# Optimization experiments

Hardware: AMD Instinct MI355X
Metric: run time of the kernel (lower is better)

Reference implementation:

```python
import jax, jax.numpy as jnp
import numpy as np

B, S, HID = 2, 2048, 2048
H, D_NOPE, D_ROPE, D_V, R = 16, 128, 64, 128, 512
D_Q = D_NOPE + D_ROPE  # 192
MAX_POS = 4096
EPS = 1e-6


def setup_inputs() -> dict:
    key = jax.random.key(0)
    ks = jax.random.split(key, 10)
    hidden_states = jax.random.normal(ks[0], (B, S, HID), dtype=jnp.float32)
    cos = jax.random.uniform(ks[1], (MAX_POS, D_ROPE // 2), dtype=jnp.float32)
    sin = jax.random.uniform(ks[2], (MAX_POS, D_ROPE // 2), dtype=jnp.float32)
    position_ids = jnp.arange(B * S, dtype=jnp.int64).reshape(B, S)
    sc = lambda d: 1.0 / np.sqrt(d)
    Wq = jax.random.normal(ks[3], (HID, H * D_Q), dtype=jnp.float32) * sc(HID)
    Wkv_a = jax.random.normal(ks[4], (HID, R + D_ROPE), dtype=jnp.float32) * sc(HID)
    ln_g = jnp.ones((R,), dtype=jnp.float32)
    ln_b = jnp.zeros((R,), dtype=jnp.float32)
    Wkv_b = jax.random.normal(ks[5], (R, H * (D_NOPE + D_V)), dtype=jnp.float32) * sc(R)
    Wo = jax.random.normal(ks[6], (H * D_V, HID), dtype=jnp.float32) * sc(H * D_V)
    return {"hidden_states": hidden_states, "cos": cos, "sin": sin,
            "position_ids": position_ids, "Wq": Wq, "Wkv_a": Wkv_a,
            "ln_g": ln_g, "ln_b": ln_b, "Wkv_b": Wkv_b, "Wo": Wo}


def _rope(t, cos, sin, position_ids):
    # t: [B,S,Hh,D_ROPE]; cos/sin: [MAX_POS, D_ROPE//2]
    c = cos[position_ids]  # [B,S,D_ROPE//2]
    s = sin[position_ids]
    c2 = jnp.concatenate([c, c], axis=-1)[:, :, None, :]  # [B,S,1,D_ROPE]
    s2 = jnp.concatenate([s, s], axis=-1)[:, :, None, :]
    half = t.shape[-1] // 2
    x1, x2 = t[..., :half], t[..., half:]
    rot = jnp.concatenate([-x2, x1], axis=-1)
    return t * c2 + rot * s2


def reference(hidden_states, cos, sin, position_ids, Wq, Wkv_a, ln_g, ln_b, Wkv_b, Wo):
    b, s, _ = hidden_states.shape
    # Q projection -> split nope/rope parts
    q = (hidden_states @ Wq).reshape(b, s, H, D_Q)
    q_nope, q_pe = q[..., :D_NOPE], q[..., D_NOPE:]
    q_pe = _rope(q_pe, cos, sin, position_ids)
    query = jnp.concatenate([q_nope, q_pe], axis=-1)  # [B,S,H,192]

    # KV latent projection
    ckv = hidden_states @ Wkv_a  # [B,S,R+D_ROPE]
    kv_c, k_pe = ckv[..., :R], ckv[..., R:]
    mu = jnp.mean(kv_c, axis=-1, keepdims=True)
    var = jnp.mean(jnp.square(kv_c - mu), axis=-1, keepdims=True)
    kv_c_n = (kv_c - mu) * jax.lax.rsqrt(var + EPS) * ln_g + ln_b
    k_pe = _rope(k_pe[:, :, None, :], cos, sin, position_ids)[:, :, 0, :]  # [B,S,64]

    # Expand latent -> per-head k_nope / v
    kv = (kv_c_n @ Wkv_b).reshape(b, s, H, D_NOPE + D_V)
    k_nope, v = kv[..., :D_NOPE], kv[..., D_NOPE:]
    key = jnp.concatenate(
        [k_nope, jnp.broadcast_to(k_pe[:, :, None, :], (b, s, H, D_ROPE))], axis=-1)

    scale = D_Q ** -0.5
    scores = jnp.einsum('bqhd,bkhd->bhqk', query, key) * scale
    causal = jnp.tril(jnp.ones((s, s), dtype=bool))
    scores = jnp.where(causal[None, None], scores, jnp.finfo(scores.dtype).min)
    attn = jax.nn.softmax(scores, axis=-1)
    out = jnp.einsum('bhqk,bkhd->bqhd', attn, v).reshape(b, s, H * D_V)
    return out @ Wo
```

## Files before the change

kernel.cpp:

```cpp
#include <hip/hip_runtime.h>
#include <math.h>
#include <stdint.h>

#define B_      2
#define S_      2048
#define HID_    2048
#define H_      16
#define D_NOPE_ 128
#define D_ROPE_ 64
#define D_V_    128
#define R_      512
#define D_Q_    192
#define NTOK    (B_ * S_)
#define EPS_    1e-6f

typedef __attribute__((ext_vector_type(8))) short bf16x8;
typedef __attribute__((ext_vector_type(4))) float f32x4;

__device__ __forceinline__ short f2bf(float x) {
    union { float f; unsigned u; } un; un.f = x;
    unsigned r = (un.u + 0x7fffu + ((un.u >> 16) & 1u)) >> 16;
    return (short)r;
}
__device__ __forceinline__ float bf2f(short s) {
    union { unsigned u; float f; } un;
    un.u = ((unsigned)(unsigned short)s) << 16;
    return un.f;
}

__device__ __forceinline__ void async_ld16(const short* gsrc, short* ldst) {
    __builtin_amdgcn_global_load_lds(
        (const __attribute__((address_space(1))) void*)gsrc,
        (__attribute__((address_space(3))) void*)ldst, 16, 0, 0);
}

#define BARX() { __builtin_amdgcn_sched_barrier(0); __builtin_amdgcn_s_barrier(); __builtin_amdgcn_sched_barrier(0); }

__global__ __launch_bounds__(256) void castk(const float* __restrict__ in, short* __restrict__ out) {
    int i = blockIdx.x * 256 + threadIdx.x;
    float4 v = ((const float4*)in)[i];
    ushort4 o;
    o.x = (unsigned short)f2bf(v.x); o.y = (unsigned short)f2bf(v.y);
    o.z = (unsigned short)f2bf(v.z); o.w = (unsigned short)f2bf(v.w);
    ((ushort4*)out)[i] = o;
}

__global__ __launch_bounds__(256) void transpose_cast(const float* __restrict__ W,
                                                      short* __restrict__ WT,
                                                      int K, int Nreal) {
    __shared__ float T[32][33];
    const int n0 = blockIdx.x * 32, k0 = blockIdx.y * 32;
    const int t = threadIdx.x;
    const int r = t >> 3, c4 = (t & 7) * 4;
    float4 v = make_float4(0.f, 0.f, 0.f, 0.f);
    if (n0 < Nreal) v = *(const float4*)&W[(size_t)(k0 + r) * Nreal + n0 + c4];
    T[r][c4 + 0] = v.x; T[r][c4 + 1] = v.y; T[r][c4 + 2] = v.z; T[r][c4 + 3] = v.w;
    __syncthreads();
    const int n = t >> 3, k4 = (t & 7) * 4;
    ushort4 o;
    o.x = (unsigned short)f2bf(T[k4 + 0][n]);
    o.y = (unsigned short)f2bf(T[k4 + 1][n]);
    o.z = (unsigned short)f2bf(T[k4 + 2][n]);
    o.w = (unsigned short)f2bf(T[k4 + 3][n]);
    *(ushort4*)&WT[(size_t)(n0 + n) * K + k0 + k4] = o;
}

template <int OUTBF>
__global__ __launch_bounds__(256) void gemm_mfma(const short* __restrict__ A,
                                                 const short* __restrict__ BT,
                                                 void* __restrict__ C,
                                                 int M, int N, int K) {
    __shared__ short As[128 * 32];
    __shared__ short Bs[128 * 32];
    const int tid = threadIdx.x;
    const int lane = tid & 63, w = tid >> 6;
    const int brow = blockIdx.y * 128, bcol = blockIdx.x * 128;

    const int o0 = w * 1024 + lane * 16;
    const int r0 = o0 >> 6, q0p = (o0 >> 4) & 3;
    const int o1 = o0 + 4096;
    const int r1 = o1 >> 6, q1p = (o1 >> 4) & 3;
    const int s0 = r0 * K + 8 * (q0p ^ ((r0 >> 1) & 3));
    const int s1 = r1 * K + 8 * (q1p ^ ((r1 >> 1) & 3));
    const short* Ab = A + (size_t)brow * K;
    const short* Bb = BT + (size_t)bcol * K;
    short* AsU0 = &As[w * 512]; short* AsU1 = &As[w * 512 + 2048];
    short* BsU0 = &Bs[w * 512]; short* BsU1 = &Bs[w * 512 + 2048];

    const int wr = w >> 1, wc = w & 1;
    const int c16 = lane & 15, g = lane >> 4;
    const int qph = (g ^ ((c16 >> 1) & 3)) * 8;

    f32x4 zero = {0.f, 0.f, 0.f, 0.f};
    f32x4 acc[4][4];
#pragma unroll
    for (int i = 0; i < 4; ++i)
#pragma unroll
        for (int j = 0; j < 4; ++j) acc[i][j] = zero;

    for (int k0 = 0; k0 < K; k0 += 32) {
        async_ld16(Ab + s0 + k0, AsU0);
        async_ld16(Ab + s1 + k0, AsU1);
        async_ld16(Bb + s0 + k0, BsU0);
        async_ld16(Bb + s1 + k0, BsU1);
        __syncthreads();
        bf16x8 af[4], bf[4];
#pragma unroll
        for (int i = 0; i < 4; ++i) {
            af[i] = *(const bf16x8*)&As[(wr * 64 + i * 16 + c16) * 32 + qph];
            bf[i] = *(const bf16x8*)&Bs[(wc * 64 + i * 16 + c16) * 32 + qph];
        }
#pragma unroll
        for (int mi = 0; mi < 4; ++mi)
#pragma unroll
            for (int ni = 0; ni < 4; ++ni)
                acc[mi][ni] = __builtin_amdgcn_mfma_f32_16x16x32_bf16(af[mi], bf[ni], acc[mi][ni], 0, 0, 0);
        __syncthreads();
    }

#pragma unroll
    for (int mi = 0; mi < 4; ++mi)
#pragma unroll
        for (int ni = 0; ni < 4; ++ni)
#pragma unroll
            for (int reg = 0; reg < 4; ++reg) {
                int row = brow + wr * 64 + mi * 16 + 4 * g + reg;
                int col = bcol + wc * 64 + ni * 16 + c16;
                if (OUTBF) ((short*)C)[(size_t)row * N + col] = f2bf(acc[mi][ni][reg]);
                else       ((float*)C)[(size_t)row * N + col] = acc[mi][ni][reg];
            }
}

template <int QA>
__global__ __launch_bounds__(512) void gemm8(const short* __restrict__ A,
                                             const short* __restrict__ BT,
                                             void* __restrict__ C0,
                                             float* __restrict__ C1,
                                             int N, int K, int nbx) {
    __shared__ short LB[2][4][8192];

    const int tid = threadIdx.x, lane = tid & 63, w = tid >> 6;
    const int c16 = lane & 15, g = lane >> 4;
    const int wr = w >> 2, wc = w & 3;
    const int qph = (g ^ ((c16 >> 1) & 3)) * 8;

    const int nwg = gridDim.x;
    const int swz = (blockIdx.x & 7) * (nwg >> 3) + (blockIdx.x >> 3);
    const int brow = (swz / nbx) * 256, bcol = (swz % nbx) * 256;

    const int o0 = w * 1024 + lane * 16;
    const int o1 = o0 + 8192;
    const int r0 = o0 >> 6, lc0 = ((o0 >> 4) & 3) ^ ((r0 >> 1) & 3);
    const int r1 = o1 >> 6, lc1 = ((o1 >> 4) & 3) ^ ((r1 >> 1) & 3);
    const short* aS0 = A + (size_t)(brow + r0) * K + lc0 * 8;
    const short* aS1 = A + (size_t)(brow + r1) * K + lc1 * 8;
    const short* bS0 = BT + (size_t)(bcol + r0) * K + lc0 * 8;
    const short* bS1 = BT + (size_t)(bcol + r1) * K + lc1 * 8;
    const int d0 = w * 512, d1 = 4096 + w * 512;

    f32x4 zero = {0.f, 0.f, 0.f, 0.f};
    f32x4 acc[8][4];
#pragma unroll
    for (int i = 0; i < 8; ++i)
#pragma unroll
        for (int j = 0; j < 4; ++j) acc[i][j] = zero;

    const int NT = K >> 6;
    async_ld16(aS0,      &LB[0][0][d0]);  async_ld16(aS1,      &LB[0][0][d1]);
    async_ld16(aS0 + 32, &LB[0][1][d0]);  async_ld16(aS1 + 32, &LB[0][1][d1]);
    async_ld16(bS0,      &LB[0][2][d0]);  async_ld16(bS1,      &LB[0][2][d1]);
    async_ld16(bS0 + 32, &LB[0][3][d0]);  async_ld16(bS1 + 32, &LB[0][3][d1]);
    asm volatile("s_waitcnt vmcnt(0)" ::: "memory");
    BARX();

    int cur = 0;
    const int arb = wr * 128, brb = wc * 64;
    for (int kt = 0; kt < NT; ++kt) {
        const bool stg = (kt + 1 < NT);
        const int ko = (kt + 1) * 64;
        short (*CB)[8192] = LB[cur];
        short (*NB)[8192] = LB[cur ^ 1];
        bf16x8 af[4], bf[4];

#pragma unroll
        for (int ni = 0; ni < 4; ++ni)
            bf[ni] = *(const bf16x8*)&CB[2][(brb + ni * 16 + c16) * 32 + qph];
#pragma unroll
        for (int mi = 0; mi < 4; ++mi)
            af[mi] = *(const bf16x8*)&CB[0][(arb + mi * 16 + c16) * 32 + qph];
        if (stg) { async_ld16(aS0 + ko, &NB[0][d0]); async_ld16(aS1 + ko, &NB[0][d1]); }
        BARX();
        __builtin_amdgcn_s_setprio(1);
#pragma unroll
        for (int mi = 0; mi < 4; ++mi)
#pragma unroll
            for (int ni = 0; ni < 4; ++ni)
                acc[mi][ni] = __builtin_amdgcn_mfma_f32_16x16x32_bf16(af[mi], bf[ni], acc[mi][ni], 0, 0, 0);
        __builtin_amdgcn_s_setprio(0);
        BARX();

#pragma unroll
        for (int mi = 0; mi < 4; ++mi)
            af[mi] = *(const bf16x8*)&CB[0][(arb + 64 + mi * 16 + c16) * 32 + qph];
        if (stg) {
            async_ld16(bS0 + ko, &NB[2][d0]); async_ld16(bS1 + ko, &NB[2][d1]);
            asm volatile("s_waitcnt vmcnt(4)" ::: "memory");
        } else {
            asm volatile("s_waitcnt vmcnt(0)" ::: "memory");
        }
        BARX();
        __builtin_amdgcn_s_setprio(1);
#pragma unroll
        for (int mi = 0; mi < 4; ++mi)
#pragma unroll
            for (int ni = 0; ni < 4; ++ni)
                acc[4 + mi][ni] = __builtin_amdgcn_mfma_f32_16x16x32_bf16(af[mi], bf[ni], acc[4 + mi][ni], 0, 0, 0);
        __builtin_amdgcn_s_setprio(0);
        BARX();

#pragma unroll
        for (int ni = 0; ni < 4; ++ni)
            bf[ni] = *(const bf16x8*)&CB[3][(brb + ni * 16 + c16) * 32 + qph];
#pragma unroll
        for (int mi = 0; mi < 4; ++mi)
            af[mi] = *(const bf16x8*)&CB[1][(arb + mi * 16 + c16) * 32 + qph];
        if (stg) { async_ld16(aS0 + ko + 32, &NB[1][d0]); async_ld16(aS1 + ko + 32, &NB[1][d1]); }
        BARX();
        __builtin_amdgcn_s_setprio(1);
#pragma unroll
        for (int mi = 0; mi < 4; ++mi)
#pragma unroll
            for (int ni = 0; ni < 4; ++ni)
                acc[mi][ni] = __builtin_amdgcn_mfma_f32_16x16x32_bf16(af[mi], bf[ni], acc[mi][ni], 0, 0, 0);
        __builtin_amdgcn_s_setprio(0);
        BARX();

#pragma unroll
        for (int mi = 0; mi < 4; ++mi)
            af[mi] = *(const bf16x8*)&CB[1][(arb + 64 + mi * 16 + c16) * 32 + qph];
        if (stg) {
            async_ld16(bS0 + ko + 32, &NB[3][d0]); async_ld16(bS1 + ko + 32, &NB[3][d1]);
            asm volatile("s_waitcnt vmcnt(4)" ::: "memory");
        }
        BARX();
        __builtin_amdgcn_s_setprio(1);
#pragma unroll
        for (int mi = 0; mi < 4; ++mi)
#pragma unroll
            for (int ni = 0; ni < 4; ++ni)
                acc[4 + mi][ni] = __builtin_amdgcn_mfma_f32_16x16x32_bf16(af[mi], bf[ni], acc[4 + mi][ni], 0, 0, 0);
        __builtin_amdgcn_s_setprio(0);
        BARX();

        cur ^= 1;
    }

    if (QA) {
        const int wcol = bcol + wc * 64;
        if (wcol < 3072) {
            short* qb = (short*)C0;
#pragma unroll
            for (int mi = 0; mi < 8; ++mi)
#pragma unroll
                for (int ni = 0; ni < 4; ++ni)
#pragma unroll
                    for (int reg = 0; reg < 4; ++reg) {
                        int row = brow + wr * 128 + mi * 16 + 4 * g + reg;
                        int col = wcol + ni * 16 + c16;
                        qb[(size_t)row * 3072 + col] = f2bf(acc[mi][ni][reg]);
                    }
        } else if (wcol < 3712) {
#pragma unroll
            for (int mi = 0; mi < 8; ++mi)
#pragma unroll
                for (int ni = 0; ni < 4; ++ni)
#pragma unroll
                    for (int reg = 0; reg < 4; ++reg) {
                        int row = brow + wr * 128 + mi * 16 + 4 * g + reg;
                        int col = wcol - 3072 + ni * 16 + c16;
                        C1[(size_t)row * 640 + col] = acc[mi][ni][reg];
                    }
        }
    } else {
        short* cc = (short*)C0;
#pragma unroll
        for (int mi = 0; mi < 8; ++mi)
#pragma unroll
            for (int ni = 0; ni < 4; ++ni)
#pragma unroll
                for (int reg = 0; reg < 4; ++reg) {
                    int row = brow + wr * 128 + mi * 16 + 4 * g + reg;
                    int col = bcol + wc * 64 + ni * 16 + c16;
                    cc[(size_t)row * N + col] = f2bf(acc[mi][ni][reg]);
                }
    }
}

__global__ __launch_bounds__(256) void rope_q_ip(short* __restrict__ qb,
                                                 const float* __restrict__ cosT,
                                                 const float* __restrict__ sinT,
                                                 const int* __restrict__ pid) {
    int gidx = blockIdx.x * 256 + threadIdx.x;
    int i = gidx & 31;
    int h = (gidx >> 5) & (H_ - 1);
    int tok = gidx >> 9;
    int pos = pid[tok];
    float c = cosT[pos * 32 + i];
    float s = sinT[pos * 32 + i];
    short* base = qb + (size_t)tok * (H_ * D_Q_) + h * D_Q_ + D_NOPE_;
    float x1 = bf2f(base[i]);
    float x2 = bf2f(base[i + 32]);
    base[i]      = f2bf(x1 * c - x2 * s);
    base[i + 32] = f2bf(x2 * c + x1 * s);
}

__global__ __launch_bounds__(256) void ln_rope(const float* __restrict__ ckv,
                                               const float* __restrict__ gam,
                                               const float* __restrict__ bet,
                                               const float* __restrict__ cosT,
                                               const float* __restrict__ sinT,
                                               const int* __restrict__ pid,
                                               short* __restrict__ kvcn,
                                               short* __restrict__ kpe) {
    const int tok = blockIdx.x, tid = threadIdx.x;
    const float* x = ckv + (size_t)tok * 640;
    float v0 = x[tid], v1 = x[tid + 256];
    float s = v0 + v1, sq = v0 * v0 + v1 * v1;
#pragma unroll
    for (int m = 1; m < 64; m <<= 1) { s += __shfl_xor(s, m); sq += __shfl_xor(sq, m); }
    __shared__ float ws[8];
    int wid = tid >> 6, lane = tid & 63;
    if (lane == 0) { ws[wid] = s; ws[4 + wid] = sq; }
    __syncthreads();
    s = ws[0] + ws[1] + ws[2] + ws[3];
    sq = ws[4] + ws[5] + ws[6] + ws[7];
    float mean = s * (1.f / 512.f);
    float var = sq * (1.f / 512.f) - mean * mean;
    float rstd = rsqrtf(var + EPS_);
    kvcn[(size_t)tok * 512 + tid]       = f2bf((v0 - mean) * rstd * gam[tid] + bet[tid]);
    kvcn[(size_t)tok * 512 + tid + 256] = f2bf((v1 - mean) * rstd * gam[tid + 256] + bet[tid + 256]);
    if (tid < 32) {
        int pos = pid[tok];
        float c = cosT[pos * 32 + tid], sn = sinT[pos * 32 + tid];
        float x1 = x[512 + tid], x2 = x[512 + 32 + tid];
        kpe[(size_t)tok * 64 + tid]      = f2bf(x1 * c - x2 * sn);
        kpe[(size_t)tok * 64 + 32 + tid] = f2bf(x2 * c + x1 * sn);
    }
}

__global__ __launch_bounds__(256) void transpose_v(const short* __restrict__ kvb,
                                                   short* __restrict__ Vt) {
    __shared__ short T[64][72];
    const int s0 = blockIdx.x * 64, d0 = blockIdx.y * 64, bh = blockIdx.z;
    const int b = bh >> 4, h = bh & 15;
    const int t = threadIdx.x;
    const int r = t >> 3, c8 = (t & 7) * 8;
#pragma unroll
    for (int i = 0; i < 2; ++i) {
        int rr = r + 32 * i;
        bf16x8 v = *(const bf16x8*)&kvb[((size_t)(b * 2048 + s0 + rr) * 16 + h) * 256 + 128 + d0 + c8];
        *(bf16x8*)&T[rr][c8] = v;
    }
    __syncthreads();
#pragma unroll
    for (int i = 0; i < 2; ++i) {
        int d = r + 32 * i;
        bf16x8 o;
#pragma unroll
        for (int j = 0; j < 8; ++j) o[j] = T[c8 + j][d];
        *(bf16x8*)&Vt[((size_t)(b * 16 + h) * 128 + d0 + d) * 2048 + s0 + c8] = o;
    }
}

__global__ __launch_bounds__(256) void flash_mfma(const short* __restrict__ qb,
                                                  const short* __restrict__ kvb,
                                                  const short* __restrict__ kpe,
                                                  const short* __restrict__ Vt,
                                                  short* __restrict__ attno) {
    __shared__ short Ks[2][64 * 128];
    __shared__ short Vs[2][128 * 64];
    __shared__ short P[4][16][72];

    const int flat = blockIdx.x;
    const int xcd = flat & 7, idx = flat >> 3;
    const int bh = xcd + 8 * (idx >> 4);
    const int pair = idx & 15;
    const int b = bh >> 4, h = bh & 15;

    const int tid = threadIdx.x, lane = tid & 63, w = tid >> 6;
    const int c16 = lane & 15, g = lane >> 4, g8 = g * 8;
    const float SC2 = 0.10412063f;

    const int o = w * 1024 + lane * 16;
    const int rK = o >> 8, ccK = ((o >> 4) & 15) ^ (rK & 7);
    const int rV = o >> 7, ccV = ((o >> 4) & 7) ^ (rV & 7);
    const short* kB0  = kvb + ((size_t)((b * 2048 + rK) * 16 + h)) * 256 + ccK * 8;
    const short* vB0  = Vt + ((size_t)((b * 16 + h) * 128 + rV)) * 2048 + ccV * 8;
    const short* peB0 = kpe + (size_t)(b * 2048 + c16) * 64 + g8;

    f32x4 zero = {0.f, 0.f, 0.f, 0.f};

#define STAGE(BUF)                                                                  \
    {                                                                               \
        _Pragma("unroll")                                                           \
        for (int rnd = 0; rnd < 4; ++rnd)                                           \
            async_ld16(kRun + (size_t)rnd * 65536,                                  \
                       &Ks[BUF][(rnd * 4096 + w * 1024) >> 1]);                     \
        _Pragma("unroll")                                                           \
        for (int rnd = 0; rnd < 4; ++rnd)                                           \
            async_ld16(vRun + (size_t)rnd * 65536,                                  \
                       &Vs[BUF][(rnd * 4096 + w * 1024) >> 1]);                     \
        kRun += 64 * 4096;                                                          \
        vRun += 64;                                                                 \
    }

    for (int half = 0; half < 2; ++half) {
        const int qt = half ? (31 - pair) : pair;
        const int q0 = qt * 64;
        const int qrow = q0 + w * 16;

        const size_t qbase = ((size_t)(b * 2048 + qrow + c16) * 16 + h) * 192 + g8;
        bf16x8 qf[6];
#pragma unroll
        for (int ks = 0; ks < 6; ++ks) qf[ks] = *(const bf16x8*)(qb + qbase + 32 * ks);

        f32x4 acc[8];
#pragma unroll
        for (int i = 0; i < 8; ++i) acc[i] = zero;
        float mreg[4] = {-INFINITY, -INFINITY, -INFINITY, -INFINITY};
        float lreg[4] = {0.f, 0.f, 0.f, 0.f};

        const short* kRun = kB0;
        const short* vRun = vB0;
        const short* peRun = peB0;

        const int nt = qt + 1;
        STAGE(0);
        __syncthreads();
        int cur = 0;

        for (int kt = 0; kt < nt; ++kt) {
            if (kt + 1 < nt) STAGE(cur ^ 1);

            f32x4 sc[4];
#pragma unroll
            for (int i = 0; i < 4; ++i) sc[i] = zero;

            __builtin_amdgcn_s_setprio(1);
#pragma unroll
            for (int ks = 0; ks < 4; ++ks)
#pragma unroll
                for (int nb = 0; nb < 4; ++nb) {
                    int row = nb * 16 + c16;
                    bf16x8 kf = *(const bf16x8*)&Ks[cur][row * 128 + (((g + 4 * ks) ^ (row & 7)) << 3)];
                    sc[nb] = __builtin_amdgcn_mfma_f32_16x16x32_bf16(qf[ks], kf, sc[nb], 0, 0, 0);
                }
#pragma unroll
            for (int ks = 0; ks < 2; ++ks)
#pragma unroll
                for (int nb = 0; nb < 4; ++nb) {
                    bf16x8 kf = *(const bf16x8*)(peRun + (size_t)nb * 16 * 64 + ks * 32);
                    sc[nb] = __builtin_amdgcn_mfma_f32_16x16x32_bf16(qf[4 + ks], kf, sc[nb], 0, 0, 0);
                }
            __builtin_amdgcn_s_setprio(0);
            peRun += 64 * 64;

            if (kt == nt - 1) {
#pragma unroll
                for (int nb = 0; nb < 4; ++nb)
#pragma unroll
                    for (int reg = 0; reg < 4; ++reg) {
                        int col = (nt - 1) * 64 + nb * 16 + c16;
                        int row = qrow + 4 * g + reg;
                        if (col > row) sc[nb][reg] = -INFINITY;
                    }
            }

            float rmax[4];
#pragma unroll
            for (int reg = 0; reg < 4; ++reg)
                rmax[reg] = fmaxf(fmaxf(sc[0][reg], sc[1][reg]), fmaxf(sc[2][reg], sc[3][reg]));
#pragma unroll
            for (int m = 1; m < 16; m <<= 1)
#pragma unroll
                for (int reg = 0; reg < 4; ++reg)
                    rmax[reg] = fmaxf(rmax[reg], __shfl_xor(rmax[reg], m));

            float grow = rmax[0] * SC2 - mreg[0];
#pragma unroll
            for (int reg = 1; reg < 4; ++reg) grow = fmaxf(grow, rmax[reg] * SC2 - mreg[reg]);
            if (__any(grow > 8.f)) {
#pragma unroll
                for (int reg = 0; reg < 4; ++reg) {
                    float mnew = fmaxf(mreg[reg], rmax[reg] * SC2);
                    float alpha = exp2f(mreg[reg] - mnew);
                    mreg[reg] = mnew;
                    lreg[reg] *= alpha;
#pragma unroll
                    for (int nb = 0; nb < 8; ++nb) acc[nb][reg] *= alpha;
                }
            }

#pragma unroll
            for (int reg = 0; reg < 4; ++reg) {
                float p0 = exp2f(fmaf(sc[0][reg], SC2, -mreg[reg]));
                float p1 = exp2f(fmaf(sc[1][reg], SC2, -mreg[reg]));
                float p2 = exp2f(fmaf(sc[2][reg], SC2, -mreg[reg]));
                float p3 = exp2f(fmaf(sc[3][reg], SC2, -mreg[reg]));
                sc[0][reg] = p0; sc[1][reg] = p1; sc[2][reg] = p2; sc[3][reg] = p3;
                lreg[reg] += (p0 + p1) + (p2 + p3);
            }

#pragma unroll
            for (int nb = 0; nb < 4; ++nb)
#pragma unroll
                for (int reg = 0; reg < 4; ++reg)
                    P[w][4 * g + reg][nb * 16 + c16] = f2bf(sc[nb][reg]);

            __builtin_amdgcn_s_setprio(1);
#pragma unroll
            for (int ks = 0; ks < 2; ++ks) {
                bf16x8 pf = *(const bf16x8*)&P[w][c16][ks * 32 + g8];
#pragma unroll
                for (int nb = 0; nb < 8; ++nb) {
                    int row = nb * 16 + c16;
                    bf16x8 vf = *(const bf16x8*)&Vs[cur][row * 64 + (((g + 4 * ks) ^ (row & 7)) << 3)];
                    acc[nb] = __builtin_amdgcn_mfma_f32_16x16x32_bf16(pf, vf, acc[nb], 0, 0, 0);
                }
            }
            __builtin_amdgcn_s_setprio(0);

            __syncthreads();
            cur ^= 1;
        }

#pragma unroll
        for (int m = 1; m < 16; m <<= 1)
#pragma unroll
            for (int reg = 0; reg < 4; ++reg)
                lreg[reg] += __shfl_xor(lreg[reg], m);
        float inv[4];
#pragma unroll
        for (int reg = 0; reg < 4; ++reg) inv[reg] = 1.f / lreg[reg];
#pragma unroll
        for (int nb = 0; nb < 8; ++nb)
#pragma unroll
            for (int reg = 0; reg < 4; ++reg)
                attno[((size_t)(b * 2048 + qrow + 4 * g + reg) * 16 + h) * 128 + nb * 16 + c16] =
                    f2bf(acc[nb][reg] * inv[reg]);
    }
#undef STAGE
}

extern "C" void kernel_launch(void* const* d_in, const int* in_sizes, int n_in,
                              void* d_out, int out_size, void* d_ws, size_t ws_size,
                              hipStream_t stream) {
    const float* hidden = (const float*)d_in[0];
    const float* cosT   = (const float*)d_in[1];
    const float* sinT   = (const float*)d_in[2];
    const int*   pid    = (const int*)d_in[3];
    const float* Wq     = (const float*)d_in[4];
    const float* Wkv_a  = (const float*)d_in[5];
    const float* ln_g   = (const float*)d_in[6];
    const float* ln_b   = (const float*)d_in[7];
    const float* Wkv_b  = (const float*)d_in[8];
    const float* Wo     = (const float*)d_in[9];
    float* out = (float*)d_out;

    char* p = (char*)d_ws;
    short* hid_bf = (short*)p;               p += (size_t)NTOK * 2048 * 2;
    short* WqkaT  = (short*)p;               p += (size_t)3840 * 2048 * 2;
    short* WkbT   = (short*)p;               p += (size_t)4096 * 512 * 2;
    short* WoT    = (short*)p;               p += (size_t)2048 * 2048 * 2;
    char*  big    = p;                       p += (size_t)NTOK * 3072 * 4;
    short* qbuf   = (short*)p;               p += (size_t)NTOK * 3072 * 2;
    short* kvcn   = (short*)p;               p += (size_t)NTOK * 512 * 2;
    short* kpe    = (short*)p;               p += (size_t)NTOK * 64 * 2;
    short* kvb    = (short*)p;               p += (size_t)NTOK * 4096 * 2;

    float* ckv   = (float*)big;
    short* Vt    = (short*)(big + (size_t)NTOK * 640 * 4);
    short* attno = (short*)(big + (size_t)NTOK * 640 * 4 + (size_t)2 * 16 * 128 * 2048 * 2);

    castk<<<8192, 256, 0, stream>>>(hidden, hid_bf);
    transpose_cast<<<dim3(96, 64), 256, 0, stream>>>(Wq, WqkaT, 2048, 3072);
    transpose_cast<<<dim3(24, 64), 256, 0, stream>>>(Wkv_a, WqkaT + (size_t)3072 * 2048, 2048, 576);
    transpose_cast<<<dim3(128, 16), 256, 0, stream>>>(Wkv_b, WkbT, 512, 4096);
    transpose_cast<<<dim3(64, 64), 256, 0, stream>>>(Wo, WoT, 2048, 2048);

    gemm8<1><<<240, 512, 0, stream>>>(hid_bf, WqkaT, qbuf, ckv, 3840, 2048, 15);
    rope_q_ip<<<(NTOK * H_ * 32) / 256, 256, 0, stream>>>(qbuf, cosT, sinT, pid);
    ln_rope<<<NTOK, 256, 0, stream>>>(ckv, ln_g, ln_b, cosT, sinT, pid, kvcn, kpe);
    gemm8<0><<<256, 512, 0, stream>>>(kvcn, WkbT, kvb, nullptr, 4096, 512, 16);
    transpose_v<<<dim3(32, 2, 32), 256, 0, stream>>>(kvb, Vt);
    flash_mfma<<<512, 256, 0, stream>>>(qbuf, kvb, kpe, Vt, attno);
    gemm_mfma<0><<<dim3(16, 32), 256, 0, stream>>>(attno, WoT, out, 4096, 2048, 2048);
}
```

Before: 308.2 us.

## Replace output-projection GEMM with double-buffered 512-thread pipelined kernel

Swaps the simple 128x128-tile, single-buffered output-projection GEMM for a new 128x256-tile kernel with 8 waves. It double-buffers LDS, prefetches the next K tile with async loads while MFMAs run, and raises wave priority around the MFMA blocks. Block indices are swizzled across the grid of 256 workgroups. The goal is to hide global-load latency and cut barrier stalls in the final GEMM, at the cost of more LDS use and a fixed layout that assumes M divisible by 128 and N by 256.

```diff
diff --git a/kernel.cpp b/kernel.cpp
--- a/kernel.cpp
+++ b/kernel.cpp
@@ -65,72 +65,6 @@
     *(ushort4*)&WT[(size_t)(n0 + n) * K + k0 + k4] = o;
 }
 
-template <int OUTBF>
-__global__ __launch_bounds__(256) void gemm_mfma(const short* __restrict__ A,
-                                                 const short* __restrict__ BT,
-                                                 void* __restrict__ C,
-                                                 int M, int N, int K) {
-    __shared__ short As[128 * 32];
-    __shared__ short Bs[128 * 32];
-    const int tid = threadIdx.x;
-    const int lane = tid & 63, w = tid >> 6;
-    const int brow = blockIdx.y * 128, bcol = blockIdx.x * 128;
-
-    const int o0 = w * 1024 + lane * 16;
-    const int r0 = o0 >> 6, q0p = (o0 >> 4) & 3;
-    const int o1 = o0 + 4096;
-    const int r1 = o1 >> 6, q1p = (o1 >> 4) & 3;
-    const int s0 = r0 * K + 8 * (q0p ^ ((r0 >> 1) & 3));
-    const int s1 = r1 * K + 8 * (q1p ^ ((r1 >> 1) & 3));
-    const short* Ab = A + (size_t)brow * K;
-    const short* Bb = BT + (size_t)bcol * K;
-    short* AsU0 = &As[w * 512]; short* AsU1 = &As[w * 512 + 2048];
-    short* BsU0 = &Bs[w * 512]; short* BsU1 = &Bs[w * 512 + 2048];
-
-    const int wr = w >> 1, wc = w & 1;
-    const int c16 = lane & 15, g = lane >> 4;
-    const int qph = (g ^ ((c16 >> 1) & 3)) * 8;
-
-    f32x4 zero = {0.f, 0.f, 0.f, 0.f};
-    f32x4 acc[4][4];
-#pragma unroll
-    for (int i = 0; i < 4; ++i)
-#pragma unroll
-        for (int j = 0; j < 4; ++j) acc[i][j] = zero;
-
-    for (int k0 = 0; k0 < K; k0 += 32) {
-        async_ld16(Ab + s0 + k0, AsU0);
-        async_ld16(Ab + s1 + k0, AsU1);
-        async_ld16(Bb + s0 + k0, BsU0);
-        async_ld16(Bb + s1 + k0, BsU1);
-        __syncthreads();
-        bf16x8 af[4], bf[4];
-#pragma unroll
-        for (int i = 0; i < 4; ++i) {
-            af[i] = *(const bf16x8*)&As[(wr * 64 + i * 16 + c16) * 32 + qph];
-            bf[i] = *(const bf16x8*)&Bs[(wc * 64 + i * 16 + c16) * 32 + qph];
-        }
-#pragma unroll
-        for (int mi = 0; mi < 4; ++mi)
-#pragma unroll
-            for (int ni = 0; ni < 4; ++ni)
-                acc[mi][ni] = __builtin_amdgcn_mfma_f32_16x16x32_bf16(af[mi], bf[ni], acc[mi][ni], 0, 0, 0);
-        __syncthreads();
-    }
-
-#pragma unroll
-    for (int mi = 0; mi < 4; ++mi)
-#pragma unroll
-        for (int ni = 0; ni < 4; ++ni)
-#pragma unroll
-            for (int reg = 0; reg < 4; ++reg) {
-                int row = brow + wr * 64 + mi * 16 + 4 * g + reg;
-                int col = bcol + wc * 64 + ni * 16 + c16;
-                if (OUTBF) ((short*)C)[(size_t)row * N + col] = f2bf(acc[mi][ni][reg]);
-                else       ((float*)C)[(size_t)row * N + col] = acc[mi][ni][reg];
-            }
-}
-
 template <int QA>
 __global__ __launch_bounds__(512) void gemm8(const short* __restrict__ A,
                                              const short* __restrict__ BT,
@@ -294,6 +228,117 @@
                     cc[(size_t)row * N + col] = f2bf(acc[mi][ni][reg]);
                 }
     }
+}
+
+__global__ __launch_bounds__(512) void gemm8n(const short* __restrict__ A,
+                                              const short* __restrict__ BT,
+                                              float* __restrict__ C,
+                                              int N, int K, int nbx) {
+    __shared__ short LA[2][2][4096];
+    __shared__ short LBt[2][2][8192];
+
+    const int tid = threadIdx.x, lane = tid & 63, w = tid >> 6;
+    const int c16 = lane & 15, g = lane >> 4;
+    const int wr = w >> 2, wc = w & 3;
+    const int qph = (g ^ ((c16 >> 1) & 3)) * 8;
+
+    const int nwg = gridDim.x;
+    const int swz = (blockIdx.x & 7) * (nwg >> 3) + (blockIdx.x >> 3);
+    const int brow = (swz / nbx) * 128, bcol = (swz % nbx) * 256;
+
+    const int oA = tid * 16;
+    const int rA = oA >> 6, lcA = ((oA >> 4) & 3) ^ ((rA >> 1) & 3);
+    const short* aS = A + (size_t)(brow + rA) * K + lcA * 8;
+    const int dA = oA >> 1;
+
+    const int o0 = w * 1024 + lane * 16, o1 = o0 + 8192;
+    const int r0 = o0 >> 6, lc0 = ((o0 >> 4) & 3) ^ ((r0 >> 1) & 3);
+    const int r1 = o1 >> 6, lc1 = ((o1 >> 4) & 3) ^ ((r1 >> 1) & 3);
+    const short* bS0 = BT + (size_t)(bcol + r0) * K + lc0 * 8;
+    const short* bS1 = BT + (size_t)(bcol + r1) * K + lc1 * 8;
+    const int d0 = o0 >> 1, d1 = o1 >> 1;
+
+    f32x4 zero = {0.f, 0.f, 0.f, 0.f};
+    f32x4 acc[4][4];
+#pragma unroll
+    for (int i = 0; i < 4; ++i)
+#pragma unroll
+        for (int j = 0; j < 4; ++j) acc[i][j] = zero;
+
+    const int NT = K >> 6;
+    async_ld16(aS,      &LA[0][0][dA]);
+    async_ld16(aS + 32, &LA[0][1][dA]);
+    async_ld16(bS0,      &LBt[0][0][d0]); async_ld16(bS1,      &LBt[0][0][d1]);
+    async_ld16(bS0 + 32, &LBt[0][1][d0]); async_ld16(bS1 + 32, &LBt[0][1][d1]);
+    asm volatile("s_waitcnt vmcnt(0)" ::: "memory");
+    BARX();
+
+    int cur = 0;
+    const int arb = wr * 64, brb = wc * 64;
+    for (int kt = 0; kt < NT; ++kt) {
+        const bool stg = (kt + 1 < NT);
+        const int ko = (kt + 1) * 64;
+        bf16x8 af[4], bf[4];
+
+#pragma unroll
+        for (int mi = 0; mi < 4; ++mi)
+            af[mi] = *(const bf16x8*)&LA[cur][0][(arb + mi * 16 + c16) * 32 + qph];
+#pragma unroll
+        for (int ni = 0; ni < 4; ++ni)
+            bf[ni] = *(const bf16x8*)&LBt[cur][0][(brb + ni * 16 + c16) * 32 + qph];
+        if (stg) {
+            async_ld16(aS + ko, &LA[cur ^ 1][0][dA]);
+            async_ld16(bS0 + ko, &LBt[cur ^ 1][0][d0]);
+            async_ld16(bS1 + ko, &LBt[cur ^ 1][0][d1]);
+            asm volatile("s_waitcnt vmcnt(3)" ::: "memory");
+        } else {
+            asm volatile("s_waitcnt vmcnt(0)" ::: "memory");
+        }
+        BARX();
+        __builtin_amdgcn_s_setprio(1);
+#pragma unroll
+        for (int mi = 0; mi < 4; ++mi)
+#pragma unroll
+            for (int ni = 0; ni < 4; ++ni)
+                acc[mi][ni] = __builtin_amdgcn_mfma_f32_16x16x32_bf16(af[mi], bf[ni], acc[mi][ni], 0, 0, 0);
+        __builtin_amdgcn_s_setprio(0);
+        BARX();
+
+#pragma unroll
+        for (int mi = 0; mi < 4; ++mi)
+            af[mi] = *(const bf16x8*)&LA[cur][1][(arb + mi * 16 + c16) * 32 + qph];
+#pragma unroll
+        for (int ni = 0; ni < 4; ++ni)
+            bf[ni] = *(const bf16x8*)&LBt[cur][1][(brb + ni * 16 + c16) * 32 + qph];
+        if (stg) {
+            async_ld16(aS + ko + 32, &LA[cur ^ 1][1][dA]);
+            async_ld16(bS0 + ko + 32, &LBt[cur ^ 1][1][d0]);
+            async_ld16(bS1 + ko + 32, &LBt[cur ^ 1][1][d1]);
+            asm volatile("s_waitcnt vmcnt(3)" ::: "memory");
+        }
+        BARX();
+        __builtin_amdgcn_s_setprio(1);
+#pragma unroll
+        for (int mi = 0; mi < 4; ++mi)
+#pragma unroll
+            for (int ni = 0; ni < 4; ++ni)
+                acc[mi][ni] = __builtin_amdgcn_mfma_f32_16x16x32_bf16(af[mi], bf[ni], acc[mi][ni], 0, 0, 0);
+        __builtin_amdgcn_s_setprio(0);
+        BARX();
+
+        cur ^= 1;
+    }
+
+#pragma unroll
+    for (int mi = 0; mi < 4; ++mi)
+#pragma unroll
+        for (int ni = 0; ni < 4; ++ni)
+#pragma unroll
+            for (int reg = 0; reg < 4; ++reg) {
+                int row = brow + wr * 64 + mi * 16 + 4 * g + reg;
+                int col = bcol + wc * 64 + ni * 16 + c16;
+                C[(size_t)row * N + col] = acc[mi][ni][reg];
+            }
 }
 
 __global__ __launch_bounds__(256) void rope_q_ip(short* __restrict__ qb,
@@ -594,5 +639,5 @@
     gemm8<0><<<256, 512, 0, stream>>>(kvcn, WkbT, kvb, nullptr, 4096, 512, 16);
     transpose_v<<<dim3(32, 2, 32), 256, 0, stream>>>(kvb, Vt);
     flash_mfma<<<512, 256, 0, stream>>>(qbuf, kvb, kpe, Vt, attno);
-    gemm_mfma<0><<<dim3(16, 32), 256, 0, stream>>>(attno, WoT, out, 4096, 2048, 2048);
-}
+    gemm8n<<<256, 512, 0, stream>>>(attno, WoT, out, 2048, 2048, 8);
+}
```

Result: faster. 297.4 us (-3.5%).
